# Kernel optimization log

Hardware: AMD Instinct MI355X
Metric: run time of the kernel (lower is better)

## Reference

```python
import jax, jax.numpy as jnp
import numpy as np

B, N, D, H, L, R = 2, 2048, 1024, 16, 3, 2
HID = int(D * 2.67)
NASH_ITERS, SINK_ITERS = 3, 10
EPS = 1e-6


def _rmsnorm(x, w):
    return x * w * jax.lax.rsqrt(jnp.mean(x * x, axis=-1, keepdims=True) + EPS)


def _sinkhorn(logits):
    # Sinkhorn-Knopp projection of exp(logits) to a doubly-stochastic matrix
    M = jnp.exp(logits)
    for _ in range(SINK_ITERS):
        M = M / jnp.sum(M, axis=1, keepdims=True)
        M = M / jnp.sum(M, axis=0, keepdims=True)
    return M


def _swiglu(x, wg, wu, wd):
    return (jax.nn.silu(x @ wg) * (x @ wu)) @ wd


def _attention(xl, wq, wk, Wv):
    # causal multi-head attention at one scale; V projection (Wv) is shared across scales
    b, n, d = xl.shape
    dh = d // H
    q = (xl @ wq).reshape(b, n, H, dh)
    k = (xl @ wk).reshape(b, n, H, dh)
    v = (xl @ Wv).reshape(b, n, H, dh)
    scores = jnp.einsum('bqhd,bkhd->bhqk', q, k) / jnp.asarray(float(np.sqrt(dh)), xl.dtype)
    mask = jnp.tril(jnp.ones((n, n), bool))
    scores = jnp.where(mask, scores, jnp.asarray(-1e9, xl.dtype))
    p = jax.nn.softmax(scores, axis=-1)
    return jnp.einsum('bhqk,bkhd->bqhd', p, v).reshape(b, n, d)


def _forward(x, norm_attn_w, norm_ffn_w, W_dec, Wq, Wk, Wv, Wo, agg_logits,
             w_gate, w_up, w_down, mhc_attn_logits, mhc_ffn_logits):
    residual = x
    xn = _rmsnorm(x, norm_attn_w)
    # 1) hierarchical decomposition: avg-pool by R each level, per-scale projection
    scales = []
    cur = xn
    for l in range(L):
        scales.append(cur @ W_dec[l])
        if l < L - 1:
            b, n, d = cur.shape
            cur = cur.reshape(b, n // R, R, d).mean(axis=2)
    # 2) multiscale causal attention with shared V; upsample back to N and project
    outs = []
    for l in range(L):
        o = _attention(scales[l], Wq[l], Wk[l], Wv)
        o = jnp.repeat(o, R ** l, axis=1)  # [B, N, D]
        outs.append(o @ Wo)
    Y = jnp.stack(outs, axis=0)  # [L, B, N, D]
    # 3) Nash aggregation: best-response iterations on scale weights
    w = jax.nn.softmax(agg_logits)
    for _ in range(NASH_ITERS):
        y_bar = jnp.einsum('l,lbnd->bnd', w, Y)
        u = -jnp.mean((Y - y_bar[None]) ** 2, axis=(1, 2, 3))  # [L] payoffs
        w = jax.nn.softmax(agg_logits + u)
    attn_out = jnp.einsum('l,lbnd->bnd', w, Y)
    aux_loss = jnp.sum(w * jnp.log(w * L + 1e-9))  # KL(w || uniform)
    # 4) mHC residual mixing (attention branch): doubly-stochastic convex mix
    P = _sinkhorn(mhc_attn_logits)
    x = P[0, 0] * residual + P[0, 1] * attn_out
    # 5) SwiGLU FFN + mHC residual (FFN branch)
    residual = x
    xn = _rmsnorm(x, norm_ffn_w)
    ffn_out = _swiglu(xn, w_gate, w_up, w_down)
    P2 = _sinkhorn(mhc_ffn_logits)
    x = P2[0, 0] * residual + P2[0, 1] * ffn_out
    return x, aux_loss


def setup_inputs() -> dict:
    key = jax.random.key(0)
    ks = jax.random.split(key, 16)
    init = 0.02
    s = lambda i, shape: jax.random.normal(ks[i], shape, jnp.float32) * init
    return {
        'x': jax.random.normal(ks[0], (B, N, D), jnp.float32),
        'norm_attn_w': jnp.ones((D,), jnp.float32),
        'norm_ffn_w': jnp.ones((D,), jnp.float32),
        'W_dec': s(1, (L, D, D)),
        'Wq': s(2, (L, D, D)),
        'Wk': s(3, (L, D, D)),
        'Wv': s(4, (D, D)),
        'Wo': s(5, (D, D)),
        'agg_logits': jnp.zeros((L,), jnp.float32),
        'w_gate': s(6, (D, HID)),
        'w_up': s(7, (D, HID)),
        'w_down': s(8, (HID, D)),
        'mhc_attn_logits': jnp.zeros((2, 2), jnp.float32),
        'mhc_ffn_logits': jnp.zeros((2, 2), jnp.float32),
    }


def reference(x, norm_attn_w, norm_ffn_w, W_dec, Wq, Wk, Wv, Wo, agg_logits,
              w_gate, w_up, w_down, mhc_attn_logits, mhc_ffn_logits):
    return _forward(x, norm_attn_w, norm_ffn_w, W_dec, Wq, Wk, Wv, Wo, agg_logits,
                    w_gate, w_up, w_down, mhc_attn_logits, mhc_ffn_logits)
```

## Files before the change

kernel.cpp:

```cpp
#include <hip/hip_runtime.h>
#include <stdint.h>


#define B_   2
#define N_   2048
#define D_   1024
#define H_   16
#define DH_  64
#define HID_ 2734
#define HIDP 2816
#define CNT  (B_*N_*D_)
#define LOG2E 1.4426950408889634f

typedef unsigned short u16;
typedef __attribute__((ext_vector_type(8))) short short8;
typedef __attribute__((ext_vector_type(4))) float f32x4;
typedef __attribute__((ext_vector_type(4))) uint16_t u16x4;

__device__ __forceinline__ u16 f2bf(float f) {
  uint32_t u = __builtin_bit_cast(uint32_t, f);
  u += 0x7fffu + ((u >> 16) & 1u);
  return (u16)(u >> 16);
}
__device__ __forceinline__ float bf2f(u16 h) {
  uint32_t u = ((uint32_t)h) << 16;
  return __builtin_bit_cast(float, u);
}
__device__ __forceinline__ uint32_t pkbf(float a, float b) {
  return (uint32_t)f2bf(a) | ((uint32_t)f2bf(b) << 16);
}
__device__ __forceinline__ void gload_lds16(const void* g, void* l) {
  __builtin_amdgcn_global_load_lds(
      (const __attribute__((address_space(1))) uint32_t*)g,
      (__attribute__((address_space(3))) uint32_t*)l, 16, 0, 0);
}

__global__ __launch_bounds__(256) void wprep_k(const float* __restrict__ Wdec, const float* __restrict__ Wq,
                                               const float* __restrict__ Wk, const float* __restrict__ Wv,
                                               const float* __restrict__ Wo, const float* __restrict__ Wg,
                                               const float* __restrict__ Wu, const float* __restrict__ Wdn,
                                               u16* __restrict__ A_wp, u16* __restrict__ WdecB,
                                               u16* __restrict__ WoT, u16* __restrict__ BTgu,
                                               u16* __restrict__ WdnT, float* __restrict__ SCb) {
  const int bid = blockIdx.x;
  if (bid >= 21760) {
    int bid0 = bid - 21760;
    int row = (bid0 < 2) ? (5454 + bid0) : (5470 + (bid0 - 2));
    u16x4 zz; zz[0]=0; zz[1]=0; zz[2]=0; zz[3]=0;
    *(u16x4*)(BTgu + (size_t)row*1024 + threadIdx.x*4) = zz;
    return;
  }
  if (bid >= 18688) {
    if (bid == 18688 && threadIdx.x < 64) SCb[threadIdx.x] = 0.f;
    int i = (bid - 18688)*1024 + threadIdx.x*4;
    float4 v = *(const float4*)(Wdec + i);
    u16x4 o; o[0]=f2bf(v.x); o[1]=f2bf(v.y); o[2]=f2bf(v.z); o[3]=f2bf(v.w);
    *(u16x4*)(WdecB + i) = o;
    return;
  }
  const float* src; u16* dst; int K, N, KP; float scale; int imode; int bx, by;
  if (bid < 9216) {
    int j = bid >> 10, t = bid & 1023; bx = t & 31; by = t >> 5;
    int l = j / 3, which = j - l*3;
    src = which==0 ? Wq + (size_t)l*1048576 : which==1 ? Wk + (size_t)l*1048576 : Wv;
    dst = A_wp + (size_t)(l*3072 + which*1024)*1024;
    K = 1024; N = 1024; KP = 1024; scale = (which==0) ? 0.125f*LOG2E : 1.f; imode = 0;
  } else if (bid < 10240) {
    int t = bid - 9216; bx = t & 31; by = t >> 5;
    src = Wo; dst = WoT; K=1024; N=1024; KP=1024; scale=1.f; imode=0;
  } else if (bid < 13056) {
    int t = bid - 10240; bx = t % 88; by = t / 88;
    src = Wg; dst = BTgu; K=1024; N=HID_; KP=1024; scale=1.f; imode=1;
  } else if (bid < 15872) {
    int t = bid - 13056; bx = t % 88; by = t / 88;
    src = Wu; dst = BTgu; K=1024; N=HID_; KP=1024; scale=1.f; imode=2;
  } else {
    int t = bid - 15872; bx = t & 31; by = t >> 5;
    src = Wdn; dst = WdnT; K=HID_; N=1024; KP=HIDP; scale=1.f; imode=0;
  }
  __shared__ float tt[32][33];
  const int tx = threadIdx.x & 31, ty = threadIdx.x >> 5;
  const int nb = bx*32, kb = by*32;
  #pragma unroll
  for (int i = 0; i < 4; i++) {
    int k = kb + ty + i*8, n = nb + tx;
    tt[ty + i*8][tx] = (k < K && n < N) ? src[(size_t)k * N + n] * scale : 0.f;
  }
  __syncthreads();
  #pragma unroll
  for (int i = 0; i < 4; i++) {
    int n = nb + ty + i*8, k = kb + tx;
    int r;
    if (imode == 0) r = n;
    else if (imode == 1) r = ((n>>4)<<5) + (n&15);
    else r = ((n>>4)<<5) + 16 + (n&15);
    dst[(size_t)r * KP + k] = f2bf(tt[tx][ty + i*8]);
  }
}

__global__ __launch_bounds__(256) void rmsA_k(const float* __restrict__ x, const float* __restrict__ w,
                                              u16* __restrict__ xn, u16* __restrict__ xp1) {
  const int j = blockIdx.x;
  const float* xr0 = x + (size_t)(2*j) * D_;
  const float* xr1 = xr0 + D_;
  float a0[4], a1[4], wv[4];
  float ss0 = 0.f, ss1 = 0.f;
  #pragma unroll
  for (int i = 0; i < 4; i++) {
    int c = threadIdx.x + i*256;
    a0[i] = xr0[c]; a1[i] = xr1[c]; wv[i] = w[c];
    ss0 += a0[i]*a0[i]; ss1 += a1[i]*a1[i];
  }
  #pragma unroll
  for (int o = 1; o < 64; o <<= 1) { ss0 += __shfl_xor(ss0, o); ss1 += __shfl_xor(ss1, o); }
  __shared__ float r0[4], r1[4];
  if ((threadIdx.x & 63) == 0) { r0[threadIdx.x >> 6] = ss0; r1[threadIdx.x >> 6] = ss1; }
  __syncthreads();
  float sc0 = rsqrtf((r0[0]+r0[1]+r0[2]+r0[3]) * (1.f/D_) + 1e-6f);
  float sc1 = rsqrtf((r1[0]+r1[1]+r1[2]+r1[3]) * (1.f/D_) + 1e-6f);
  #pragma unroll
  for (int i = 0; i < 4; i++) {
    int c = threadIdx.x + i*256;
    float xa = a0[i]*wv[i]*sc0, xb = a1[i]*wv[i]*sc1;
    xn[(size_t)(2*j)*D_ + c]     = f2bf(xa);
    xn[(size_t)(2*j)*D_ + D_ + c] = f2bf(xb);
    xp1[(size_t)j*D_ + c] = f2bf(0.5f*(xa + xb));
  }
}

__global__ __launch_bounds__(256) void pool_k(const u16* __restrict__ in, u16* __restrict__ out, int lg) {
  const int No = 1 << lg;
  const int total4 = B_ * No * 256;
  for (int i = blockIdx.x*256 + threadIdx.x; i < total4; i += gridDim.x*256) {
    int d4 = i & 255; int j = (i >> 8) & (No - 1); int b = i >> (8 + lg);
    size_t src = ((size_t)(b*2*No + 2*j) << 10) + d4*4;
    u16x4 a = *(const u16x4*)(in + src);
    u16x4 c = *(const u16x4*)(in + src + 1024);
    u16x4 o;
    #pragma unroll
    for (int t = 0; t < 4; t++) o[t] = f2bf(0.5f * (bf2f(a[t]) + bf2f(c[t])));
    *(u16x4*)(out + (size_t)i*4) = o;
  }
}

template<int MT, int MODE>
__global__ __launch_bounds__(256, 2) void gemm_t(const u16* __restrict__ A, const u16* __restrict__ BT,
                                                 void* __restrict__ Cv, void* __restrict__ Cv2,
                                                 const float* __restrict__ X1,
                                                 const float* __restrict__ SCp,
                                                 int N, int K, int t1, int t2, unsigned int bt_stride) {
  static_assert(MT == 4, "counted vmcnt(8) assumes MT+4 == 8 staging loads");
  __shared__ __align__(16) u16 As[2][MT*32*64];
  __shared__ __align__(16) u16 Bs[2][128*64];
  const int tid = threadIdx.x;
  const int lane = tid & 63, wid = tid >> 6;
  const int quad = lane >> 4, c16 = lane & 15;
  const int y = blockIdx.y;
  const int m0 = y * (MT*32), n0 = blockIdx.x * 128;
  const int wm = wid >> 1, wn = wid & 1;
  const int level = (y >= t2) ? 2 : ((y >= t1) ? 1 : 0);
  BT += (size_t)level * bt_stride;

  f32x4 acc[MT][4];
  #pragma unroll
  for (int i = 0; i < MT; i++)
    #pragma unroll
    for (int j = 0; j < 4; j++) acc[i][j] = f32x4{0.f,0.f,0.f,0.f};

  const int srow = lane >> 3;
  const int schunk = lane & 7;
  auto stage = [&](int k0, int p) {
    #pragma unroll
    for (int t = 0; t < MT; t++) {
      int idx = wid*MT + t;
      int row = idx*8 + srow;
      int g = (schunk ^ (row & 7)) * 8;
      gload_lds16(A + (size_t)(m0+row)*K + k0 + g, &As[p][idx*512]);
    }
    #pragma unroll
    for (int t = 0; t < 4; t++) {
      int idx = wid*4 + t;
      int row = idx*8 + srow;
      int g = (schunk ^ (row & 7)) * 8;
      gload_lds16(BT + (size_t)(n0+row)*K + k0 + g, &Bs[p][idx*512]);
    }
  };

  const int nk = K >> 6;
  stage(0, 0);
  for (int ki = 0; ki < nk; ki++) {
    const int p = ki & 1;
    if (ki + 1 < nk) {
      stage((ki + 1) << 6, p ^ 1);
      asm volatile("s_waitcnt vmcnt(8)" ::: "memory");
    } else {
      asm volatile("s_waitcnt vmcnt(0)" ::: "memory");
    }
    __builtin_amdgcn_s_barrier();
    __builtin_amdgcn_sched_barrier(0);
    __builtin_amdgcn_s_setprio(1);
    #pragma unroll
    for (int kh = 0; kh < 2; kh++) {
      short8 af[MT], bfr[4];
      #pragma unroll
      for (int mt = 0; mt < MT; mt++) {
        int ar = wm*(MT*16) + mt*16 + c16;
        int ck = (kh*4 + quad) ^ (ar & 7);
        af[mt] = *(const short8*)(&As[p][ar*64 + ck*8]);
      }
      #pragma unroll
      for (int nt = 0; nt < 4; nt++) {
        int br = wn*64 + nt*16 + c16;
        int ck = (kh*4 + quad) ^ (br & 7);
        bfr[nt] = *(const short8*)(&Bs[p][br*64 + ck*8]);
      }
      #pragma unroll
      for (int mt = 0; mt < MT; mt++)
        #pragma unroll
        for (int nt = 0; nt < 4; nt++)
          acc[mt][nt] = __builtin_amdgcn_mfma_f32_16x16x32_bf16(af[mt], bfr[nt], acc[mt][nt], 0, 0, 0);
    }
    __builtin_amdgcn_s_setprio(0);
    __builtin_amdgcn_sched_barrier(0);
    __builtin_amdgcn_s_barrier();
  }
  if (MODE == 1) {
    u16* C = (u16*)Cv;
    #pragma unroll
    for (int mt = 0; mt < MT; mt++)
      #pragma unroll
      for (int nt = 0; nt < 4; nt++)
        #pragma unroll
        for (int r = 0; r < 4; r++) {
          int row = m0 + wm*(MT*16) + mt*16 + quad*4 + r;
          int col = n0 + wn*64 + nt*16 + c16;
          C[(size_t)row * N + col] = f2bf(acc[mt][nt][r]);
        }
  } else if (MODE == 2) {
    float* C = (float*)Cv;
    const float q0 = SCp[11], q1 = SCp[12];
    #pragma unroll
    for (int mt = 0; mt < MT; mt++)
      #pragma unroll
      for (int nt = 0; nt < 4; nt++)
        #pragma unroll
        for (int r = 0; r < 4; r++) {
          int row = m0 + wm*(MT*16) + mt*16 + quad*4 + r;
          int col = n0 + wn*64 + nt*16 + c16;
          size_t o = (size_t)row * N + col;
          C[o] = q0 * X1[o] + q1 * acc[mt][nt][r];
        }
  } else if (MODE == 3) {
    u16* Hc = (u16*)Cv;
    const int hbase = (n0 >> 1) + wn*32;
    #pragma unroll
    for (int mt = 0; mt < MT; mt++)
      #pragma unroll
      for (int r = 0; r < 4; r++) {
        int row = m0 + wm*(MT*16) + mt*16 + quad*4 + r;
        #pragma unroll
        for (int pr = 0; pr < 2; pr++) {
          float g = acc[mt][2*pr][r], u = acc[mt][2*pr+1][r];
          float h = g / (1.f + __expf(-g)) * u;
          Hc[(size_t)row * HIDP + hbase + pr*16 + c16] = f2bf(h);
        }
      }
  } else {
    if (n0 < 2048) {
      u16* C = (u16*)Cv;
      #pragma unroll
      for (int mt = 0; mt < MT; mt++)
        #pragma unroll
        for (int nt = 0; nt < 4; nt++)
          #pragma unroll
          for (int r = 0; r < 4; r++) {
            int row = m0 + wm*(MT*16) + mt*16 + quad*4 + r;
            int col = n0 + wn*64 + nt*16 + c16;
            C[(size_t)row * N + col] = f2bf(acc[mt][nt][r]);
          }
    } else {
      const int Nl = 2048 >> level;
      const int lvbase = (level==0) ? 0 : (level==1) ? 4096 : 6144;
      const size_t vtoff = (level==0) ? 0 : (level==1) ? 4194304 : 6291456;
      u16* VT = (u16*)Cv2 + vtoff;
      #pragma unroll
      for (int mt = 0; mt < MT; mt++) {
        int rowg = m0 + wm*(MT*16) + mt*16 + quad*4;
        int nloc = rowg - lvbase;
        int b = nloc / Nl;
        int n = nloc - b*Nl;
        #pragma unroll
        for (int nt = 0; nt < 4; nt++) {
          int c = n0 - 2048 + wn*64 + nt*16 + c16;
          u16x4 o;
          o[0]=f2bf(acc[mt][nt][0]); o[1]=f2bf(acc[mt][nt][1]);
          o[2]=f2bf(acc[mt][nt][2]); o[3]=f2bf(acc[mt][nt][3]);
          *(u16x4*)(VT + ((size_t)(b*1024 + c))*Nl + n) = o;
        }
      }
    }
  }
}

__global__ __launch_bounds__(256) void flash_k(const u16* __restrict__ QKVg,
                                               const u16* __restrict__ VTg,
                                               u16* __restrict__ Og) {
  __shared__ __align__(16) u16 Kt[2][64*64];
  __shared__ __align__(16) u16 Vt[2][64*64];
  __shared__ __align__(16) u16 Ps[4][32*68];
  const int tid = threadIdx.x, lane = tid & 63, wid = tid >> 6;
  const int quad = lane >> 4, c16 = lane & 15;
  const int id = blockIdx.x;
  int qt, bh, Nl, rowbase; size_t vtoff;
  if (id < 512)      { qt = 15 - (id >> 5);            bh = id & 31;  Nl = 2048; rowbase = 0;    vtoff = 0; }
  else if (id < 768) { int t2 = id - 512; qt = 7 - (t2 >> 5); bh = t2 & 31; Nl = 1024; rowbase = 4096; vtoff = 4194304; }
  else               { int t2 = id - 768; qt = 3 - (t2 >> 5); bh = t2 & 31; Nl = 512;  rowbase = 6144; vtoff = 6291456; }
  const int b = bh >> 4, h = bh & 15;
  const u16* QK = QKVg + ((size_t)(rowbase + b*Nl)) * 3072 + h*64;
  u16* Ow = Og + ((size_t)(rowbase + b*Nl)) * 1024 + h*64;
  const u16* VT = VTg + vtoff + ((size_t)b*1024 + h*64) * (size_t)Nl;

  const int q0r = qt*128 + wid*32;
  short8 bq[2][2];
  #pragma unroll
  for (int qh = 0; qh < 2; qh++) {
    const u16* qp = QK + (size_t)(q0r + qh*16 + c16)*3072 + quad*8;
    bq[qh][0] = *(const short8*)qp;
    bq[qh][1] = *(const short8*)(qp + 32);
  }
  const int si0 = wid*2, si1 = si0 + 1;
  const int sr0 = si0*8 + (lane>>3), sr1 = si1*8 + (lane>>3);
  const int sg  = ((lane&7) ^ (lane>>3)) * 8;
  const u16* Ks0 = QK + 1024 + (size_t)sr0*3072 + sg;
  const u16* Ks1 = QK + 1024 + (size_t)sr1*3072 + sg;
  const u16* Vs0 = VT + (size_t)sr0*Nl + sg;
  const u16* Vs1 = VT + (size_t)sr1*Nl + sg;

  f32x4 oacc[2][4];
  f32x4 lacc[2];
  #pragma unroll
  for (int qh = 0; qh < 2; qh++) {
    lacc[qh] = f32x4{0.f,0.f,0.f,0.f};
    #pragma unroll
    for (int nt = 0; nt < 4; nt++) oacc[qh][nt] = f32x4{0.f,0.f,0.f,0.f};
  }

  auto stage = [&](int kt, int p) {
    const size_t ko = (size_t)kt * 64;
    gload_lds16(Ks0 + ko*3072, &Kt[p][si0*512]);
    gload_lds16(Ks1 + ko*3072, &Kt[p][si1*512]);
    gload_lds16(Vs0 + ko,      &Vt[p][si0*512]);
    gload_lds16(Vs1 + ko,      &Vt[p][si1*512]);
  };
  const int kmax_w = 2*qt + (wid >> 1);
  const int ktot   = 2*qt + 2;
  stage(0, 0);

  for (int kt = 0; kt < ktot; kt++) {
    const int p = kt & 1;
    __syncthreads();
    if (kt + 1 < ktot) stage(kt+1, p^1);
    if (kt > kmax_w) continue;

    f32x4 st[2][4];
    #pragma unroll
    for (int nt = 0; nt < 4; nt++) {
      int key = nt*16 + c16, x = key & 7;
      short8 a0 = *(const short8*)(&Kt[p][key*64 + ((quad    ) ^ x)*8]);
      short8 a1 = *(const short8*)(&Kt[p][key*64 + ((quad + 4) ^ x)*8]);
      #pragma unroll
      for (int qh = 0; qh < 2; qh++) {
        f32x4 s = f32x4{0.f,0.f,0.f,0.f};
        s = __builtin_amdgcn_mfma_f32_16x16x32_bf16(a0, bq[qh][0], s, 0, 0, 0);
        s = __builtin_amdgcn_mfma_f32_16x16x32_bf16(a1, bq[qh][1], s, 0, 0, 0);
        st[qh][nt] = s;
      }
    }
    if (kt >= 2*qt) {
      const int kb = kt*64;
      #pragma unroll
      for (int qh = 0; qh < 2; qh++) {
        const int qr = q0r + qh*16 + c16;
        #pragma unroll
        for (int nt = 0; nt < 4; nt++) {
          #pragma unroll
          for (int r = 0; r < 4; r++) {
            float e = __builtin_amdgcn_exp2f(st[qh][nt][r]);
            st[qh][nt][r] = (kb + nt*16 + quad*4 + r <= qr) ? e : 0.f;
          }
          lacc[qh] += st[qh][nt];
        }
      }
    } else {
      #pragma unroll
      for (int qh = 0; qh < 2; qh++)
        #pragma unroll
        for (int nt = 0; nt < 4; nt++) {
          #pragma unroll
          for (int r = 0; r < 4; r++) st[qh][nt][r] = __builtin_amdgcn_exp2f(st[qh][nt][r]);
          lacc[qh] += st[qh][nt];
        }
    }
    #pragma unroll
    for (int qh = 0; qh < 2; qh++) {
      const int prow = qh*16 + c16;
      #pragma unroll
      for (int nt = 0; nt < 4; nt++) {
        uint2 pk;
        pk.x = pkbf(st[qh][nt][0], st[qh][nt][1]);
        pk.y = pkbf(st[qh][nt][2], st[qh][nt][3]);
        *(uint2*)(&Ps[wid][prow*68 + nt*16 + quad*4]) = pk;
      }
    }
    short8 bp[2][2];
    #pragma unroll
    for (int qh = 0; qh < 2; qh++) {
      bp[qh][0] = *(const short8*)(&Ps[wid][(qh*16 + c16)*68 +      quad*8]);
      bp[qh][1] = *(const short8*)(&Ps[wid][(qh*16 + c16)*68 + 32 + quad*8]);
    }
    #pragma unroll
    for (int nt = 0; nt < 4; nt++) {
      int dh = nt*16 + c16, x = dh & 7;
      short8 a0 = *(const short8*)(&Vt[p][dh*64 + ((quad    ) ^ x)*8]);
      short8 a1 = *(const short8*)(&Vt[p][dh*64 + ((quad + 4) ^ x)*8]);
      #pragma unroll
      for (int qh = 0; qh < 2; qh++) {
        oacc[qh][nt] = __builtin_amdgcn_mfma_f32_16x16x32_bf16(a0, bp[qh][0], oacc[qh][nt], 0, 0, 0);
        oacc[qh][nt] = __builtin_amdgcn_mfma_f32_16x16x32_bf16(a1, bp[qh][1], oacc[qh][nt], 0, 0, 0);
      }
    }
  }
  #pragma unroll
  for (int qh = 0; qh < 2; qh++) {
    float ls = lacc[qh][0] + lacc[qh][1] + lacc[qh][2] + lacc[qh][3];
    ls += __shfl_xor(ls, 16);
    ls += __shfl_xor(ls, 32);
    const float rl = 1.f / ls;
    #pragma unroll
    for (int nt = 0; nt < 4; nt++) {
      uint2 o;
      o.x = pkbf(oacc[qh][nt][0]*rl, oacc[qh][nt][1]*rl);
      o.y = pkbf(oacc[qh][nt][2]*rl, oacc[qh][nt][3]*rl);
      *(uint2*)(Ow + (size_t)(q0r + qh*16 + c16)*1024 + nt*16 + quad*4) = o;
    }
  }
}

__global__ __launch_bounds__(256) void gram_k(const u16* __restrict__ Y0, const u16* __restrict__ Y1,
                                              const u16* __restrict__ Y2, float* __restrict__ G) {
  float a[6] = {0,0,0,0,0,0};
  const int total4 = CNT/4;
  for (int i = blockIdx.x*256 + threadIdx.x; i < total4; i += gridDim.x*256) {
    int d4 = i & 255; int n = (i >> 8) & (N_-1); int b = i >> 19;
    u16x4 y0v = *(const u16x4*)(Y0 + (size_t)i*4);
    u16x4 y1v = *(const u16x4*)(Y1 + (((size_t)(b*1024 + (n>>1))) << 10) + d4*4);
    u16x4 y2v = *(const u16x4*)(Y2 + (((size_t)(b*512  + (n>>2))) << 10) + d4*4);
    #pragma unroll
    for (int t = 0; t < 4; t++) {
      float y0 = bf2f(y0v[t]), y1 = bf2f(y1v[t]), y2 = bf2f(y2v[t]);
      a[0] += y0*y0; a[1] += y0*y1; a[2] += y0*y2;
      a[3] += y1*y1; a[4] += y1*y2; a[5] += y2*y2;
    }
  }
  __shared__ float red[4][6];
  const int lane = threadIdx.x & 63, wid = threadIdx.x >> 6;
  #pragma unroll
  for (int t = 0; t < 6; t++) {
    float v = a[t];
    v += __shfl_xor(v, 1);  v += __shfl_xor(v, 2);  v += __shfl_xor(v, 4);
    v += __shfl_xor(v, 8);  v += __shfl_xor(v, 16); v += __shfl_xor(v, 32);
    a[t] = v;
  }
  if (lane == 0)
    #pragma unroll
    for (int t = 0; t < 6; t++) red[wid][t] = a[t];
  __syncthreads();
  if (threadIdx.x < 6)
    atomicAdd(&G[threadIdx.x], red[0][threadIdx.x] + red[1][threadIdx.x] +
                               red[2][threadIdx.x] + red[3][threadIdx.x]);
}

__global__ void head_k(float* SC, const float* __restrict__ agg, const float* __restrict__ mA,
                       const float* __restrict__ mF, float* __restrict__ aux_out) {
  if (threadIdx.x != 0 || blockIdx.x != 0) return;
  float G[6];
  for (int t = 0; t < 6; t++) G[t] = SC[t];
  const int gi[3][3] = {{0,1,2},{1,3,4},{2,4,5}};
  float a[3] = {agg[0], agg[1], agg[2]};
  float w[3];
  {
    float m = fmaxf(a[0], fmaxf(a[1], a[2])); float s = 0.f;
    for (int l = 0; l < 3; l++) { w[l] = expf(a[l]-m); s += w[l]; }
    for (int l = 0; l < 3; l++) w[l] /= s;
  }
  const float inv = 1.f / (float)CNT;
  for (int it = 0; it < 3; it++) {
    float q = 0.f;
    for (int l = 0; l < 3; l++) for (int m2 = 0; m2 < 3; m2++) q += w[l]*w[m2]*G[gi[l][m2]];
    float z[3];
    for (int l = 0; l < 3; l++) {
      float dot = w[0]*G[gi[l][0]] + w[1]*G[gi[l][1]] + w[2]*G[gi[l][2]];
      z[l] = a[l] - (G[gi[l][l]] - 2.f*dot + q) * inv;
    }
    float m = fmaxf(z[0], fmaxf(z[1], z[2])); float s = 0.f;
    for (int l = 0; l < 3; l++) { w[l] = expf(z[l]-m); s += w[l]; }
    for (int l = 0; l < 3; l++) w[l] /= s;
  }
  SC[6] = w[0]; SC[7] = w[1]; SC[8] = w[2];
  aux_out[0] = w[0]*logf(w[0]*3.f + 1e-9f) + w[1]*logf(w[1]*3.f + 1e-9f) + w[2]*logf(w[2]*3.f + 1e-9f);
  for (int which = 0; which < 2; which++) {
    const float* Lg = which ? mF : mA;
    float M0 = expf(Lg[0]), M1 = expf(Lg[1]), M2 = expf(Lg[2]), M3 = expf(Lg[3]);
    for (int i2 = 0; i2 < 10; i2++) {
      float r0 = M0+M1, r1 = M2+M3; M0 /= r0; M1 /= r0; M2 /= r1; M3 /= r1;
      float c0 = M0+M2, c1 = M1+M3; M0 /= c0; M2 /= c0; M1 /= c1; M3 /= c1;
    }
    SC[9 + which*2] = M0; SC[10 + which*2] = M1;
  }
}

__global__ __launch_bounds__(256) void mixrms_k(const float* __restrict__ x, const u16* __restrict__ Y0,
                                                const u16* __restrict__ Y1, const u16* __restrict__ Y2,
                                                const float* __restrict__ SC, const float* __restrict__ w2,
                                                float* __restrict__ x1, u16* __restrict__ xn2) {
  const float w0 = SC[6], w1 = SC[7], ww2 = SC[8], p0 = SC[9], p1 = SC[10];
  const int i = blockIdx.x;
  const int b = i >> 11, n = i & 2047;
  const float* xr = x + (size_t)i * D_;
  const u16* y0 = Y0 + (size_t)i * D_;
  const u16* y1 = Y1 + (size_t)(b*1024 + (n>>1)) * D_;
  const u16* y2 = Y2 + (size_t)(b*512  + (n>>2)) * D_;
  float xv[4], wv[4];
  float ss = 0.f;
  #pragma unroll
  for (int t = 0; t < 4; t++) {
    int c = threadIdx.x + t*256;
    float v = p0*xr[c] + p1*(w0*bf2f(y0[c]) + w1*bf2f(y1[c]) + ww2*bf2f(y2[c]));
    xv[t] = v; wv[t] = w2[c]; ss += v*v;
    x1[(size_t)i*D_ + c] = v;
  }
  #pragma unroll
  for (int o = 1; o < 64; o <<= 1) ss += __shfl_xor(ss, o);
  __shared__ float red[4];
  if ((threadIdx.x & 63) == 0) red[threadIdx.x >> 6] = ss;
  __syncthreads();
  float sc = rsqrtf((red[0]+red[1]+red[2]+red[3]) * (1.f/D_) + 1e-6f);
  #pragma unroll
  for (int t = 0; t < 4; t++) {
    int c = threadIdx.x + t*256;
    xn2[(size_t)i*D_ + c] = f2bf(xv[t]*wv[t]*sc);
  }
}

extern "C" void kernel_launch(void* const* d_in, const int* in_sizes, int n_in,
                              void* d_out, int out_size, void* d_ws, size_t ws_size,
                              hipStream_t stream) {
  (void)in_sizes; (void)n_in; (void)out_size; (void)ws_size;
  const float* x    = (const float*)d_in[0];
  const float* nw1  = (const float*)d_in[1];
  const float* nw2  = (const float*)d_in[2];
  const float* Wdec = (const float*)d_in[3];
  const float* Wq   = (const float*)d_in[4];
  const float* Wk   = (const float*)d_in[5];
  const float* Wv   = (const float*)d_in[6];
  const float* Wo   = (const float*)d_in[7];
  const float* agg  = (const float*)d_in[8];
  const float* Wg   = (const float*)d_in[9];
  const float* Wu   = (const float*)d_in[10];
  const float* Wdn  = (const float*)d_in[11];
  const float* mA   = (const float*)d_in[12];
  const float* mF   = (const float*)d_in[13];
  float* out = (float*)d_out;

  char* ws = (char*)d_ws;
  size_t off = 0;
  auto take = [&](size_t b) { size_t r = off; off += (b + 255) & ~(size_t)255; return r; };

  u16* A_wp  = (u16*)(ws + take((size_t)9216*1024*2));
  u16* WdecB = (u16*)(ws + take((size_t)3*1024*1024*2));
  u16* Wqkv  = (u16*)(ws + take((size_t)9216*1024*2));
  u16* BTgu  = (u16*)(ws + take((size_t)5632*1024*2));
  u16* WdnT  = (u16*)(ws + take((size_t)HIDP*1024*2));
  u16* WoT   = (u16*)(ws + take((size_t)1024*1024*2));
  u16* xn_all = (u16*)(ws + take((size_t)7168*1024*2));
  float* x1  = (float*)(ws + take((size_t)CNT*4));
  float* SCb = (float*)(ws + take(256));
  char*  big = ws + take(88080384);
  u16*   QKV   = (u16*)big;
  u16*   VTa   = (u16*)(big + 44040192);
  u16*   Ob    = (u16*)(big + 58720256);
  u16*   YC    = (u16*)(big + 73400320);
  u16*   hbuf  = (u16*)big;

  dim3 blk(256);
  const int BIG = 1 << 30;

  wprep_k<<<21924, blk, 0, stream>>>(Wdec, Wq, Wk, Wv, Wo, Wg, Wu, Wdn,
                                     A_wp, WdecB, WoT, BTgu, WdnT, SCb);
  gemm_t<4,1><<<dim3(8, 72), blk, 0, stream>>>(A_wp, WdecB, Wqkv, nullptr, nullptr, nullptr,
                                               1024, 1024, 24, 48, 1024u*1024u);
  rmsA_k<<<2048, blk, 0, stream>>>(x, nw1, xn_all, xn_all + (size_t)4096*1024);
  pool_k<<<512, blk, 0, stream>>>(xn_all + (size_t)4096*1024, xn_all + (size_t)6144*1024, 9);
  gemm_t<4,4><<<dim3(24, 56), blk, 0, stream>>>(xn_all, Wqkv, QKV, VTa, nullptr, nullptr,
                                                3072, 1024, 32, 48, 3072u*1024u);
  flash_k<<<896, blk, 0, stream>>>(QKV, VTa, Ob);
  gemm_t<4,1><<<dim3(8, 56), blk, 0, stream>>>(Ob, WoT, YC, nullptr, nullptr, nullptr,
                                               1024, 1024, BIG, BIG, 0u);
  u16* YC1 = YC + (size_t)4096*1024;
  u16* YC2 = YC + (size_t)6144*1024;
  gram_k<<<1024, blk, 0, stream>>>(YC, YC1, YC2, SCb);
  head_k<<<1, 64, 0, stream>>>(SCb, agg, mA, mF, out + CNT);
  mixrms_k<<<4096, blk, 0, stream>>>(x, YC, YC1, YC2, SCb, nw2, x1, xn_all);
  gemm_t<4,3><<<dim3(44, 32), blk, 0, stream>>>(xn_all, BTgu, hbuf, nullptr, nullptr, nullptr,
                                                5632, 1024, BIG, BIG, 0u);
  gemm_t<4,2><<<dim3(8, 32), blk, 0, stream>>>(hbuf, WdnT, out, nullptr, x1, SCb,
                                               1024, HIDP, BIG, BIG, 0u);
}
```

Measured before the change: 494.1 us.

## Add 512-thread 256x128-tile GEMM kernel with split-stage prefetch for bf16 outputs

```diff
diff --git a/kernel.cpp b/kernel.cpp
--- a/kernel.cpp
+++ b/kernel.cpp
@@ -143,121 +143,110 @@
   }
 }
 
-template<int MT, int MODE>
-__global__ __launch_bounds__(256, 2) void gemm_t(const u16* __restrict__ A, const u16* __restrict__ BT,
-                                                 void* __restrict__ Cv, void* __restrict__ Cv2,
-                                                 const float* __restrict__ X1,
-                                                 const float* __restrict__ SCp,
-                                                 int N, int K, int t1, int t2, unsigned int bt_stride) {
-  static_assert(MT == 4, "counted vmcnt(8) assumes MT+4 == 8 staging loads");
-  __shared__ __align__(16) u16 As[2][MT*32*64];
-  __shared__ __align__(16) u16 Bs[2][128*64];
+template<int MODE>
+__global__ __launch_bounds__(512) void gemm8_t(const u16* __restrict__ A, const u16* __restrict__ BT,
+                                               void* __restrict__ Cv, void* __restrict__ Cv2,
+                                               int N, int K, int t1, int t2, unsigned int bt_stride) {
+  extern __shared__ __align__(16) u16 smem[];
+  u16* As = smem;
+  u16* Bs = smem + 2*16384;
   const int tid = threadIdx.x;
   const int lane = tid & 63, wid = tid >> 6;
   const int quad = lane >> 4, c16 = lane & 15;
   const int y = blockIdx.y;
-  const int m0 = y * (MT*32), n0 = blockIdx.x * 128;
+  const int m0 = y * 256, n0 = blockIdx.x * 128;
   const int wm = wid >> 1, wn = wid & 1;
   const int level = (y >= t2) ? 2 : ((y >= t1) ? 1 : 0);
   BT += (size_t)level * bt_stride;
 
-  f32x4 acc[MT][4];
-  #pragma unroll
-  for (int i = 0; i < MT; i++)
+  f32x4 acc[4][4];
+  #pragma unroll
+  for (int i = 0; i < 4; i++)
     #pragma unroll
     for (int j = 0; j < 4; j++) acc[i][j] = f32x4{0.f,0.f,0.f,0.f};
 
   const int srow = lane >> 3;
   const int schunk = lane & 7;
-  auto stage = [&](int k0, int p) {
-    #pragma unroll
-    for (int t = 0; t < MT; t++) {
-      int idx = wid*MT + t;
-      int row = idx*8 + srow;
-      int g = (schunk ^ (row & 7)) * 8;
-      gload_lds16(A + (size_t)(m0+row)*K + k0 + g, &As[p][idx*512]);
-    }
+  auto stageA = [&](int k0, int p) {
     #pragma unroll
     for (int t = 0; t < 4; t++) {
       int idx = wid*4 + t;
       int row = idx*8 + srow;
       int g = (schunk ^ (row & 7)) * 8;
-      gload_lds16(BT + (size_t)(n0+row)*K + k0 + g, &Bs[p][idx*512]);
+      gload_lds16(A + (size_t)(m0+row)*K + k0 + g, As + p*16384 + idx*512);
     }
   };
+  auto stageB = [&](int k0, int p) {
+    #pragma unroll
+    for (int t = 0; t < 2; t++) {
+      int idx = wid*2 + t;
+      int row = idx*8 + srow;
+      int g = (schunk ^ (row & 7)) * 8;
+      gload_lds16(BT + (size_t)(n0+row)*K + k0 + g, Bs + p*8192 + idx*512);
+    }
+  };
 
   const int nk = K >> 6;
-  stage(0, 0);
-  for (int ki = 0; ki < nk; ki++) {
-    const int p = ki & 1;
-    if (ki + 1 < nk) {
-      stage((ki + 1) << 6, p ^ 1);
-      asm volatile("s_waitcnt vmcnt(8)" ::: "memory");
-    } else {
-      asm volatile("s_waitcnt vmcnt(0)" ::: "memory");
-    }
-    __builtin_amdgcn_s_barrier();
-    __builtin_amdgcn_sched_barrier(0);
-    __builtin_amdgcn_s_setprio(1);
-    #pragma unroll
-    for (int kh = 0; kh < 2; kh++) {
-      short8 af[MT], bfr[4];
-      #pragma unroll
-      for (int mt = 0; mt < MT; mt++) {
-        int ar = wm*(MT*16) + mt*16 + c16;
+  stageA(0, 0); stageB(0, 0);
+  asm volatile("s_waitcnt vmcnt(0)" ::: "memory");
+  __builtin_amdgcn_s_barrier();
+  for (int k = 0; k < nk; ++k) {
+    const int p = k & 1;
+    #pragma unroll
+    for (int kh = 0; kh < 2; ++kh) {
+      short8 af[4], bf[4];
+      #pragma unroll
+      for (int i = 0; i < 4; i++) {
+        int ar = wm*64 + i*16 + c16;
         int ck = (kh*4 + quad) ^ (ar & 7);
-        af[mt] = *(const short8*)(&As[p][ar*64 + ck*8]);
+        af[i] = *(const short8*)(As + p*16384 + ar*64 + ck*8);
       }
       #pragma unroll
       for (int nt = 0; nt < 4; nt++) {
         int br = wn*64 + nt*16 + c16;
         int ck = (kh*4 + quad) ^ (br & 7);
-        bfr[nt] = *(const short8*)(&Bs[p][br*64 + ck*8]);
-      }
-      #pragma unroll
-      for (int mt = 0; mt < MT; mt++)
+        bf[nt] = *(const short8*)(Bs + p*8192 + br*64 + ck*8);
+      }
+      if (k + 1 < nk) {
+        if (kh == 0) stageA((k+1) << 6, p ^ 1);
+        else         stageB((k+1) << 6, p ^ 1);
+      }
+      __builtin_amdgcn_s_barrier();
+      __builtin_amdgcn_sched_barrier(0);
+      __builtin_amdgcn_s_setprio(1);
+      #pragma unroll
+      for (int i = 0; i < 4; i++)
         #pragma unroll
         for (int nt = 0; nt < 4; nt++)
-          acc[mt][nt] = __builtin_amdgcn_mfma_f32_16x16x32_bf16(af[mt], bfr[nt], acc[mt][nt], 0, 0, 0);
-    }
-    __builtin_amdgcn_s_setprio(0);
-    __builtin_amdgcn_sched_barrier(0);
-    __builtin_amdgcn_s_barrier();
-  }
+          acc[i][nt] = __builtin_amdgcn_mfma_f32_16x16x32_bf16(af[i], bf[nt], acc[i][nt], 0, 0, 0);
+      __builtin_amdgcn_s_setprio(0);
+      __builtin_amdgcn_sched_barrier(0);
+      if (kh == 1 && k + 1 < nk)
+        asm volatile("s_waitcnt vmcnt(0)" ::: "memory");
+      __builtin_amdgcn_s_barrier();
+    }
+  }
+  const int rbase = m0 + wm*64;
   if (MODE == 1) {
     u16* C = (u16*)Cv;
     #pragma unroll
-    for (int mt = 0; mt < MT; mt++)
+    for (int mt = 0; mt < 4; mt++)
       #pragma unroll
       for (int nt = 0; nt < 4; nt++)
         #pragma unroll
         for (int r = 0; r < 4; r++) {
-          int row = m0 + wm*(MT*16) + mt*16 + quad*4 + r;
+          int row = rbase + mt*16 + quad*4 + r;
           int col = n0 + wn*64 + nt*16 + c16;
           C[(size_t)row * N + col] = f2bf(acc[mt][nt][r]);
-        }
-  } else if (MODE == 2) {
-    float* C = (float*)Cv;
-    const float q0 = SCp[11], q1 = SCp[12];
-    #pragma unroll
-    for (int mt = 0; mt < MT; mt++)
-      #pragma unroll
-      for (int nt = 0; nt < 4; nt++)
-        #pragma unroll
-        for (int r = 0; r < 4; r++) {
-          int row = m0 + wm*(MT*16) + mt*16 + quad*4 + r;
-          int col = n0 + wn*64 + nt*16 + c16;
-          size_t o = (size_t)row * N + col;
-          C[o] = q0 * X1[o] + q1 * acc[mt][nt][r];
         }
   } else if (MODE == 3) {
     u16* Hc = (u16*)Cv;
     const int hbase = (n0 >> 1) + wn*32;
     #pragma unroll
-    for (int mt = 0; mt < MT; mt++)
+    for (int mt = 0; mt < 4; mt++)
       #pragma unroll
       for (int r = 0; r < 4; r++) {
-        int row = m0 + wm*(MT*16) + mt*16 + quad*4 + r;
+        int row = rbase + mt*16 + quad*4 + r;
         #pragma unroll
         for (int pr = 0; pr < 2; pr++) {
           float g = acc[mt][2*pr][r], u = acc[mt][2*pr+1][r];
@@ -269,12 +258,12 @@
     if (n0 < 2048) {
       u16* C = (u16*)Cv;
       #pragma unroll
-      for (int mt = 0; mt < MT; mt++)
+      for (int mt = 0; mt < 4; mt++)
         #pragma unroll
         for (int nt = 0; nt < 4; nt++)
           #pragma unroll
           for (int r = 0; r < 4; r++) {
-            int row = m0 + wm*(MT*16) + mt*16 + quad*4 + r;
+            int row = rbase + mt*16 + quad*4 + r;
             int col = n0 + wn*64 + nt*16 + c16;
             C[(size_t)row * N + col] = f2bf(acc[mt][nt][r]);
           }
@@ -284,8 +273,8 @@
       const size_t vtoff = (level==0) ? 0 : (level==1) ? 4194304 : 6291456;
       u16* VT = (u16*)Cv2 + vtoff;
       #pragma unroll
-      for (int mt = 0; mt < MT; mt++) {
-        int rowg = m0 + wm*(MT*16) + mt*16 + quad*4;
+      for (int mt = 0; mt < 4; mt++) {
+        int rowg = rbase + mt*16 + quad*4;
         int nloc = rowg - lvbase;
         int b = nloc / Nl;
         int n = nloc - b*Nl;
@@ -300,6 +289,100 @@
       }
     }
   }
+}
+
+template<int MT, int MODE>
+__global__ __launch_bounds__(256, 2) void gemm_t(const u16* __restrict__ A, const u16* __restrict__ BT,
+                                                 void* __restrict__ Cv,
+                                                 const float* __restrict__ X1,
+                                                 const float* __restrict__ SCp,
+                                                 int N, int K) {
+  static_assert(MT == 4, "counted vmcnt(8) assumes MT+4 == 8 staging loads");
+  __shared__ __align__(16) u16 As[2][MT*32*64];
+  __shared__ __align__(16) u16 Bs[2][128*64];
+  const int tid = threadIdx.x;
+  const int lane = tid & 63, wid = tid >> 6;
+  const int quad = lane >> 4, c16 = lane & 15;
+  const int y = blockIdx.y;
+  const int m0 = y * (MT*32), n0 = blockIdx.x * 128;
+  const int wm = wid >> 1, wn = wid & 1;
+
+  f32x4 acc[MT][4];
+  #pragma unroll
+  for (int i = 0; i < MT; i++)
+    #pragma unroll
+    for (int j = 0; j < 4; j++) acc[i][j] = f32x4{0.f,0.f,0.f,0.f};
+
+  const int srow = lane >> 3;
+  const int schunk = lane & 7;
+  auto stage = [&](int k0, int p) {
+    #pragma unroll
+    for (int t = 0; t < MT; t++) {
+      int idx = wid*MT + t;
+      int row = idx*8 + srow;
+      int g = (schunk ^ (row & 7)) * 8;
+      gload_lds16(A + (size_t)(m0+row)*K + k0 + g, &As[p][idx*512]);
+    }
+    #pragma unroll
+    for (int t = 0; t < 4; t++) {
+      int idx = wid*4 + t;
+      int row = idx*8 + srow;
+      int g = (schunk ^ (row & 7)) * 8;
+      gload_lds16(BT + (size_t)(n0+row)*K + k0 + g, &Bs[p][idx*512]);
+    }
+  };
+
+  const int nk = K >> 6;
+  stage(0, 0);
+  for (int ki = 0; ki < nk; ki++) {
+    const int p = ki & 1;
+    if (ki + 1 < nk) {
+      stage((ki + 1) << 6, p ^ 1);
+      asm volatile("s_waitcnt vmcnt(8)" ::: "memory");
+    } else {
+      asm volatile("s_waitcnt vmcnt(0)" ::: "memory");
+    }
+    __builtin_amdgcn_s_barrier();
+    __builtin_amdgcn_sched_barrier(0);
+    __builtin_amdgcn_s_setprio(1);
+    #pragma unroll
+    for (int kh = 0; kh < 2; kh++) {
+      short8 af[MT], bfr[4];
+      #pragma unroll
+      for (int mt = 0; mt < MT; mt++) {
+        int ar = wm*(MT*16) + mt*16 + c16;
+        int ck = (kh*4 + quad) ^ (ar & 7);
+        af[mt] = *(const short8*)(&As[p][ar*64 + ck*8]);
+      }
+      #pragma unroll
+      for (int nt = 0; nt < 4; nt++) {
+        int br = wn*64 + nt*16 + c16;
+        int ck = (kh*4 + quad) ^ (br & 7);
+        bfr[nt] = *(const short8*)(&Bs[p][br*64 + ck*8]);
+      }
+      #pragma unroll
+      for (int mt = 0; mt < MT; mt++)
+        #pragma unroll
+        for (int nt = 0; nt < 4; nt++)
+          acc[mt][nt] = __builtin_amdgcn_mfma_f32_16x16x32_bf16(af[mt], bfr[nt], acc[mt][nt], 0, 0, 0);
+    }
+    __builtin_amdgcn_s_setprio(0);
+    __builtin_amdgcn_sched_barrier(0);
+    __builtin_amdgcn_s_barrier();
+  }
+  float* C = (float*)Cv;
+  const float q0 = SCp[11], q1 = SCp[12];
+  #pragma unroll
+  for (int mt = 0; mt < MT; mt++)
+    #pragma unroll
+    for (int nt = 0; nt < 4; nt++)
+      #pragma unroll
+      for (int r = 0; r < 4; r++) {
+        int row = m0 + wm*(MT*16) + mt*16 + quad*4 + r;
+        int col = n0 + wn*64 + nt*16 + c16;
+        size_t o = (size_t)row * N + col;
+        C[o] = q0 * X1[o] + q1 * acc[mt][nt][r];
+      }
 }
 
 __global__ __launch_bounds__(256) void flash_k(const u16* __restrict__ QKVg,
@@ -594,25 +677,26 @@
 
   dim3 blk(256);
   const int BIG = 1 << 30;
+  const size_t SM8 = 98304;
 
   wprep_k<<<21924, blk, 0, stream>>>(Wdec, Wq, Wk, Wv, Wo, Wg, Wu, Wdn,
                                      A_wp, WdecB, WoT, BTgu, WdnT, SCb);
-  gemm_t<4,1><<<dim3(8, 72), blk, 0, stream>>>(A_wp, WdecB, Wqkv, nullptr, nullptr, nullptr,
-                                               1024, 1024, 24, 48, 1024u*1024u);
+  gemm8_t<1><<<dim3(8, 36), 512, SM8, stream>>>(A_wp, WdecB, Wqkv, nullptr,
+                                                1024, 1024, 12, 24, 1024u*1024u);
   rmsA_k<<<2048, blk, 0, stream>>>(x, nw1, xn_all, xn_all + (size_t)4096*1024);
   pool_k<<<512, blk, 0, stream>>>(xn_all + (size_t)4096*1024, xn_all + (size_t)6144*1024, 9);
-  gemm_t<4,4><<<dim3(24, 56), blk, 0, stream>>>(xn_all, Wqkv, QKV, VTa, nullptr, nullptr,
-                                                3072, 1024, 32, 48, 3072u*1024u);
+  gemm8_t<4><<<dim3(24, 28), 512, SM8, stream>>>(xn_all, Wqkv, QKV, VTa,
+                                                 3072, 1024, 16, 24, 3072u*1024u);
   flash_k<<<896, blk, 0, stream>>>(QKV, VTa, Ob);
-  gemm_t<4,1><<<dim3(8, 56), blk, 0, stream>>>(Ob, WoT, YC, nullptr, nullptr, nullptr,
-                                               1024, 1024, BIG, BIG, 0u);
+  gemm8_t<1><<<dim3(8, 28), 512, SM8, stream>>>(Ob, WoT, YC, nullptr,
+                                                1024, 1024, BIG, BIG, 0u);
   u16* YC1 = YC + (size_t)4096*1024;
   u16* YC2 = YC + (size_t)6144*1024;
   gram_k<<<1024, blk, 0, stream>>>(YC, YC1, YC2, SCb);
   head_k<<<1, 64, 0, stream>>>(SCb, agg, mA, mF, out + CNT);
   mixrms_k<<<4096, blk, 0, stream>>>(x, YC, YC1, YC2, SCb, nw2, x1, xn_all);
-  gemm_t<4,3><<<dim3(44, 32), blk, 0, stream>>>(xn_all, BTgu, hbuf, nullptr, nullptr, nullptr,
-                                                5632, 1024, BIG, BIG, 0u);
-  gemm_t<4,2><<<dim3(8, 32), blk, 0, stream>>>(hbuf, WdnT, out, nullptr, x1, SCb,
-                                               1024, HIDP, BIG, BIG, 0u);
-}
+  gemm8_t<3><<<dim3(44, 16), 512, SM8, stream>>>(xn_all, BTgu, hbuf, nullptr,
+                                                 5632, 1024, BIG, BIG, 0u);
+  gemm_t<4,2><<<dim3(8, 32), blk, 0, stream>>>(hbuf, WdnT, out, x1, SCb,
+                                               1024, HIDP);
+}
```

New measurement: 512.9 us. +3.8%, slower.

## Make GEMMs persistent with atomic tile tickets; use smaller M tile for down-proj

Applied to the files above, without the earlier changes.

```diff
diff --git a/kernel.cpp b/kernel.cpp
--- a/kernel.cpp
+++ b/kernel.cpp
@@ -144,129 +144,98 @@
 }
 
 template<int MT, int MODE>
-__global__ __launch_bounds__(256, 2) void gemm_t(const u16* __restrict__ A, const u16* __restrict__ BT,
+__global__ __launch_bounds__(256, 2) void gemm_p(const u16* __restrict__ A, const u16* __restrict__ BT,
                                                  void* __restrict__ Cv, void* __restrict__ Cv2,
                                                  const float* __restrict__ X1,
                                                  const float* __restrict__ SCp,
+                                                 int* __restrict__ ticket,
+                                                 int nx, int ntiles,
                                                  int N, int K, int t1, int t2, unsigned int bt_stride) {
-  static_assert(MT == 4, "counted vmcnt(8) assumes MT+4 == 8 staging loads");
   __shared__ __align__(16) u16 As[2][MT*32*64];
   __shared__ __align__(16) u16 Bs[2][128*64];
+  __shared__ int tsh;
   const int tid = threadIdx.x;
   const int lane = tid & 63, wid = tid >> 6;
   const int quad = lane >> 4, c16 = lane & 15;
-  const int y = blockIdx.y;
-  const int m0 = y * (MT*32), n0 = blockIdx.x * 128;
   const int wm = wid >> 1, wn = wid & 1;
-  const int level = (y >= t2) ? 2 : ((y >= t1) ? 1 : 0);
-  BT += (size_t)level * bt_stride;
-
-  f32x4 acc[MT][4];
-  #pragma unroll
-  for (int i = 0; i < MT; i++)
-    #pragma unroll
-    for (int j = 0; j < 4; j++) acc[i][j] = f32x4{0.f,0.f,0.f,0.f};
-
   const int srow = lane >> 3;
   const int schunk = lane & 7;
-  auto stage = [&](int k0, int p) {
-    #pragma unroll
-    for (int t = 0; t < MT; t++) {
-      int idx = wid*MT + t;
-      int row = idx*8 + srow;
-      int g = (schunk ^ (row & 7)) * 8;
-      gload_lds16(A + (size_t)(m0+row)*K + k0 + g, &As[p][idx*512]);
-    }
-    #pragma unroll
-    for (int t = 0; t < 4; t++) {
-      int idx = wid*4 + t;
-      int row = idx*8 + srow;
-      int g = (schunk ^ (row & 7)) * 8;
-      gload_lds16(BT + (size_t)(n0+row)*K + k0 + g, &Bs[p][idx*512]);
-    }
-  };
-
-  const int nk = K >> 6;
-  stage(0, 0);
-  for (int ki = 0; ki < nk; ki++) {
-    const int p = ki & 1;
-    if (ki + 1 < nk) {
-      stage((ki + 1) << 6, p ^ 1);
-      asm volatile("s_waitcnt vmcnt(8)" ::: "memory");
-    } else {
-      asm volatile("s_waitcnt vmcnt(0)" ::: "memory");
-    }
-    __builtin_amdgcn_s_barrier();
-    __builtin_amdgcn_sched_barrier(0);
-    __builtin_amdgcn_s_setprio(1);
-    #pragma unroll
-    for (int kh = 0; kh < 2; kh++) {
-      short8 af[MT], bfr[4];
-      #pragma unroll
-      for (int mt = 0; mt < MT; mt++) {
-        int ar = wm*(MT*16) + mt*16 + c16;
-        int ck = (kh*4 + quad) ^ (ar & 7);
-        af[mt] = *(const short8*)(&As[p][ar*64 + ck*8]);
-      }
-      #pragma unroll
-      for (int nt = 0; nt < 4; nt++) {
-        int br = wn*64 + nt*16 + c16;
-        int ck = (kh*4 + quad) ^ (br & 7);
-        bfr[nt] = *(const short8*)(&Bs[p][br*64 + ck*8]);
-      }
-      #pragma unroll
-      for (int mt = 0; mt < MT; mt++)
-        #pragma unroll
-        for (int nt = 0; nt < 4; nt++)
-          acc[mt][nt] = __builtin_amdgcn_mfma_f32_16x16x32_bf16(af[mt], bfr[nt], acc[mt][nt], 0, 0, 0);
-    }
-    __builtin_amdgcn_s_setprio(0);
-    __builtin_amdgcn_sched_barrier(0);
-    __builtin_amdgcn_s_barrier();
-  }
-  if (MODE == 1) {
-    u16* C = (u16*)Cv;
-    #pragma unroll
-    for (int mt = 0; mt < MT; mt++)
-      #pragma unroll
-      for (int nt = 0; nt < 4; nt++)
-        #pragma unroll
-        for (int r = 0; r < 4; r++) {
-          int row = m0 + wm*(MT*16) + mt*16 + quad*4 + r;
-          int col = n0 + wn*64 + nt*16 + c16;
-          C[(size_t)row * N + col] = f2bf(acc[mt][nt][r]);
+
+  for (;;) {
+    if (tid == 0) tsh = atomicAdd(ticket, 1);
+    __syncthreads();
+    const int tile = tsh;
+    __syncthreads();
+    if (tile >= ntiles) break;
+    const int by = tile / nx;
+    const int bx = tile - by * nx;
+    const int m0 = by * (MT*32), n0 = bx * 128;
+    const int level = (by >= t2) ? 2 : ((by >= t1) ? 1 : 0);
+    const u16* BTl = BT + (size_t)level * bt_stride;
+
+    f32x4 acc[MT][4];
+    #pragma unroll
+    for (int i = 0; i < MT; i++)
+      #pragma unroll
+      for (int j = 0; j < 4; j++) acc[i][j] = f32x4{0.f,0.f,0.f,0.f};
+
+    auto stage = [&](int k0, int p) {
+      #pragma unroll
+      for (int t = 0; t < MT; t++) {
+        int idx = wid*MT + t;
+        int row = idx*8 + srow;
+        int g = (schunk ^ (row & 7)) * 8;
+        gload_lds16(A + (size_t)(m0+row)*K + k0 + g, &As[p][idx*512]);
+      }
+      #pragma unroll
+      for (int t = 0; t < 4; t++) {
+        int idx = wid*4 + t;
+        int row = idx*8 + srow;
+        int g = (schunk ^ (row & 7)) * 8;
+        gload_lds16(BTl + (size_t)(n0+row)*K + k0 + g, &Bs[p][idx*512]);
+      }
+    };
+
+    const int nk = K >> 6;
+    stage(0, 0);
+    for (int ki = 0; ki < nk; ki++) {
+      const int p = ki & 1;
+      if (ki + 1 < nk) {
+        stage((ki + 1) << 6, p ^ 1);
+        if constexpr (MT == 4) asm volatile("s_waitcnt vmcnt(8)" ::: "memory");
+        else                   asm volatile("s_waitcnt vmcnt(6)" ::: "memory");
+      } else {
+        asm volatile("s_waitcnt vmcnt(0)" ::: "memory");
+      }
+      __builtin_amdgcn_s_barrier();
+      __builtin_amdgcn_sched_barrier(0);
+      __builtin_amdgcn_s_setprio(1);
+      #pragma unroll
+      for (int kh = 0; kh < 2; kh++) {
+        short8 af[MT], bfr[4];
+        #pragma unroll
+        for (int mt = 0; mt < MT; mt++) {
+          int ar = wm*(MT*16) + mt*16 + c16;
+          int ck = (kh*4 + quad) ^ (ar & 7);
+          af[mt] = *(const short8*)(&As[p][ar*64 + ck*8]);
         }
-  } else if (MODE == 2) {
-    float* C = (float*)Cv;
-    const float q0 = SCp[11], q1 = SCp[12];
-    #pragma unroll
-    for (int mt = 0; mt < MT; mt++)
-      #pragma unroll
-      for (int nt = 0; nt < 4; nt++)
-        #pragma unroll
-        for (int r = 0; r < 4; r++) {
-          int row = m0 + wm*(MT*16) + mt*16 + quad*4 + r;
-          int col = n0 + wn*64 + nt*16 + c16;
-          size_t o = (size_t)row * N + col;
-          C[o] = q0 * X1[o] + q1 * acc[mt][nt][r];
+        #pragma unroll
+        for (int nt = 0; nt < 4; nt++) {
+          int br = wn*64 + nt*16 + c16;
+          int ck = (kh*4 + quad) ^ (br & 7);
+          bfr[nt] = *(const short8*)(&Bs[p][br*64 + ck*8]);
         }
-  } else if (MODE == 3) {
-    u16* Hc = (u16*)Cv;
-    const int hbase = (n0 >> 1) + wn*32;
-    #pragma unroll
-    for (int mt = 0; mt < MT; mt++)
-      #pragma unroll
-      for (int r = 0; r < 4; r++) {
-        int row = m0 + wm*(MT*16) + mt*16 + quad*4 + r;
-        #pragma unroll
-        for (int pr = 0; pr < 2; pr++) {
-          float g = acc[mt][2*pr][r], u = acc[mt][2*pr+1][r];
-          float h = g / (1.f + __expf(-g)) * u;
-          Hc[(size_t)row * HIDP + hbase + pr*16 + c16] = f2bf(h);
-        }
-      }
-  } else {
-    if (n0 < 2048) {
+        #pragma unroll
+        for (int mt = 0; mt < MT; mt++)
+          #pragma unroll
+          for (int nt = 0; nt < 4; nt++)
+            acc[mt][nt] = __builtin_amdgcn_mfma_f32_16x16x32_bf16(af[mt], bfr[nt], acc[mt][nt], 0, 0, 0);
+      }
+      __builtin_amdgcn_s_setprio(0);
+      __builtin_amdgcn_sched_barrier(0);
+      __builtin_amdgcn_s_barrier();
+    }
+    if (MODE == 1) {
       u16* C = (u16*)Cv;
       #pragma unroll
       for (int mt = 0; mt < MT; mt++)
@@ -278,24 +247,67 @@
             int col = n0 + wn*64 + nt*16 + c16;
             C[(size_t)row * N + col] = f2bf(acc[mt][nt][r]);
           }
+    } else if (MODE == 2) {
+      float* C = (float*)Cv;
+      const float q0 = SCp[11], q1 = SCp[12];
+      #pragma unroll
+      for (int mt = 0; mt < MT; mt++)
+        #pragma unroll
+        for (int nt = 0; nt < 4; nt++)
+          #pragma unroll
+          for (int r = 0; r < 4; r++) {
+            int row = m0 + wm*(MT*16) + mt*16 + quad*4 + r;
+            int col = n0 + wn*64 + nt*16 + c16;
+            size_t o = (size_t)row * N + col;
+            C[o] = q0 * X1[o] + q1 * acc[mt][nt][r];
+          }
+    } else if (MODE == 3) {
+      u16* Hc = (u16*)Cv;
+      const int hbase = (n0 >> 1) + wn*32;
+      #pragma unroll
+      for (int mt = 0; mt < MT; mt++)
+        #pragma unroll
+        for (int r = 0; r < 4; r++) {
+          int row = m0 + wm*(MT*16) + mt*16 + quad*4 + r;
+          #pragma unroll
+          for (int pr = 0; pr < 2; pr++) {
+            float g = acc[mt][2*pr][r], u = acc[mt][2*pr+1][r];
+            float h = g / (1.f + __expf(-g)) * u;
+            Hc[(size_t)row * HIDP + hbase + pr*16 + c16] = f2bf(h);
+          }
+        }
     } else {
-      const int Nl = 2048 >> level;
-      const int lvbase = (level==0) ? 0 : (level==1) ? 4096 : 6144;
-      const size_t vtoff = (level==0) ? 0 : (level==1) ? 4194304 : 6291456;
-      u16* VT = (u16*)Cv2 + vtoff;
-      #pragma unroll
-      for (int mt = 0; mt < MT; mt++) {
-        int rowg = m0 + wm*(MT*16) + mt*16 + quad*4;
-        int nloc = rowg - lvbase;
-        int b = nloc / Nl;
-        int n = nloc - b*Nl;
-        #pragma unroll
-        for (int nt = 0; nt < 4; nt++) {
-          int c = n0 - 2048 + wn*64 + nt*16 + c16;
-          u16x4 o;
-          o[0]=f2bf(acc[mt][nt][0]); o[1]=f2bf(acc[mt][nt][1]);
-          o[2]=f2bf(acc[mt][nt][2]); o[3]=f2bf(acc[mt][nt][3]);
-          *(u16x4*)(VT + ((size_t)(b*1024 + c))*Nl + n) = o;
+      if (n0 < 2048) {
+        u16* C = (u16*)Cv;
+        #pragma unroll
+        for (int mt = 0; mt < MT; mt++)
+          #pragma unroll
+          for (int nt = 0; nt < 4; nt++)
+            #pragma unroll
+            for (int r = 0; r < 4; r++) {
+              int row = m0 + wm*(MT*16) + mt*16 + quad*4 + r;
+              int col = n0 + wn*64 + nt*16 + c16;
+              C[(size_t)row * N + col] = f2bf(acc[mt][nt][r]);
+            }
+      } else {
+        const int Nl = 2048 >> level;
+        const int lvbase = (level==0) ? 0 : (level==1) ? 4096 : 6144;
+        const size_t vtoff = (level==0) ? 0 : (level==1) ? 4194304 : 6291456;
+        u16* VT = (u16*)Cv2 + vtoff;
+        #pragma unroll
+        for (int mt = 0; mt < MT; mt++) {
+          int rowg = m0 + wm*(MT*16) + mt*16 + quad*4;
+          int nloc = rowg - lvbase;
+          int b = nloc / Nl;
+          int n = nloc - b*Nl;
+          #pragma unroll
+          for (int nt = 0; nt < 4; nt++) {
+            int c = n0 - 2048 + wn*64 + nt*16 + c16;
+            u16x4 o;
+            o[0]=f2bf(acc[mt][nt][0]); o[1]=f2bf(acc[mt][nt][1]);
+            o[2]=f2bf(acc[mt][nt][2]); o[3]=f2bf(acc[mt][nt][3]);
+            *(u16x4*)(VT + ((size_t)(b*1024 + c))*Nl + n) = o;
+          }
         }
       }
     }
@@ -592,27 +604,29 @@
   u16*   YC    = (u16*)(big + 73400320);
   u16*   hbuf  = (u16*)big;
 
+  int* tk = (int*)SCb + 16;
+
   dim3 blk(256);
   const int BIG = 1 << 30;
 
   wprep_k<<<21924, blk, 0, stream>>>(Wdec, Wq, Wk, Wv, Wo, Wg, Wu, Wdn,
                                      A_wp, WdecB, WoT, BTgu, WdnT, SCb);
-  gemm_t<4,1><<<dim3(8, 72), blk, 0, stream>>>(A_wp, WdecB, Wqkv, nullptr, nullptr, nullptr,
-                                               1024, 1024, 24, 48, 1024u*1024u);
+  gemm_p<4,1><<<512, blk, 0, stream>>>(A_wp, WdecB, Wqkv, nullptr, nullptr, nullptr,
+                                       tk + 0, 8, 576, 1024, 1024, 24, 48, 1024u*1024u);
   rmsA_k<<<2048, blk, 0, stream>>>(x, nw1, xn_all, xn_all + (size_t)4096*1024);
   pool_k<<<512, blk, 0, stream>>>(xn_all + (size_t)4096*1024, xn_all + (size_t)6144*1024, 9);
-  gemm_t<4,4><<<dim3(24, 56), blk, 0, stream>>>(xn_all, Wqkv, QKV, VTa, nullptr, nullptr,
-                                                3072, 1024, 32, 48, 3072u*1024u);
+  gemm_p<4,4><<<512, blk, 0, stream>>>(xn_all, Wqkv, QKV, VTa, nullptr, nullptr,
+                                       tk + 1, 24, 1344, 3072, 1024, 32, 48, 3072u*1024u);
   flash_k<<<896, blk, 0, stream>>>(QKV, VTa, Ob);
-  gemm_t<4,1><<<dim3(8, 56), blk, 0, stream>>>(Ob, WoT, YC, nullptr, nullptr, nullptr,
-                                               1024, 1024, BIG, BIG, 0u);
+  gemm_p<4,1><<<448, blk, 0, stream>>>(Ob, WoT, YC, nullptr, nullptr, nullptr,
+                                       tk + 2, 8, 448, 1024, 1024, BIG, BIG, 0u);
   u16* YC1 = YC + (size_t)4096*1024;
   u16* YC2 = YC + (size_t)6144*1024;
   gram_k<<<1024, blk, 0, stream>>>(YC, YC1, YC2, SCb);
   head_k<<<1, 64, 0, stream>>>(SCb, agg, mA, mF, out + CNT);
   mixrms_k<<<4096, blk, 0, stream>>>(x, YC, YC1, YC2, SCb, nw2, x1, xn_all);
-  gemm_t<4,3><<<dim3(44, 32), blk, 0, stream>>>(xn_all, BTgu, hbuf, nullptr, nullptr, nullptr,
-                                                5632, 1024, BIG, BIG, 0u);
-  gemm_t<4,2><<<dim3(8, 32), blk, 0, stream>>>(hbuf, WdnT, out, nullptr, x1, SCb,
-                                               1024, HIDP, BIG, BIG, 0u);
-}
+  gemm_p<4,3><<<512, blk, 0, stream>>>(xn_all, BTgu, hbuf, nullptr, nullptr, nullptr,
+                                       tk + 3, 44, 1408, 5632, 1024, BIG, BIG, 0u);
+  gemm_p<2,2><<<512, blk, 0, stream>>>(hbuf, WdnT, out, nullptr, x1, SCb,
+                                       tk + 4, 8, 512, 1024, HIDP, BIG, BIG, 0u);
+}
```

Measured after the change: 507.4 us. 1.03x slower.
